# Kernel optimization log

Hardware: AMD Instinct MI355X
Metric: run time of the kernel (lower is better)

Reference implementation:

```python
import jax, jax.numpy as jnp
import numpy as np

NUM_HEADS = 16
D_K = 8  # == n_qubits


def setup_inputs() -> dict:
    key = jax.random.key(0)
    k1, k2, k3 = jax.random.split(key, 3)
    x = jax.random.normal(k1, (4, 2048, 128), dtype=jnp.float32)
    # trainable RX angles, one per qubit (tq.RX has_params=True)
    theta = jax.random.normal(k2, (D_K,), dtype=jnp.float32)
    # out_proj: Linear(embed_dim, embed_dim, bias=False)
    w_out = jax.random.normal(k3, (128, 128), dtype=jnp.float32) * (1.0 / np.sqrt(128.0))
    return {"x": x, "theta": theta, "w_out": w_out}


def quantum_features(x, theta):
    # x: [b, s, e]. Per head of size d_k: encode RX(x_i), trainable RX(theta_i)
    # (composes to RX(x_i + theta_i)), CNOT ladder [i, i+1], measure PauliZ.
    # Heisenberg picture: Z_w -> Z_0...Z_w, so <Z_w> = prod_{i<=w} cos(x_i + theta_i).
    b, s, e = x.shape
    heads = x.reshape(b, s, NUM_HEADS, D_K)
    return jnp.cumprod(jnp.cos(heads + theta), axis=-1)  # [b, s, h, d_k]


def reference(x, theta, w_out):
    b, s, e = x.shape
    # q == k == v: same shared q_layer applied to the same x three times.
    qkv = quantum_features(x, theta)            # [b, s, h, d_k]
    q = qkv.transpose(0, 2, 1, 3)               # [b, h, s, d_k]
    scores = jnp.einsum('bhqd,bhkd->bhqk', q, q) / np.sqrt(D_K)
    attn = jax.nn.softmax(scores, axis=-1)      # dropout is identity at eval
    out = jnp.einsum('bhqk,bhkd->bhqd', attn, q)
    out = out.transpose(0, 2, 1, 3).reshape(b, s, e)
    return out @ w_out.T
```

## Files before the change

kernel.cpp:

```cpp
#include <hip/hip_runtime.h>

#define BATCH 4
#define SEQ   2048
#define EMB   128
#define NH    16
#define DK    8

#define QSCALE 0.510069726f

typedef _Float16 v4h __attribute__((ext_vector_type(4)));
typedef _Float16 v8h __attribute__((ext_vector_type(8)));
typedef float    v4f __attribute__((ext_vector_type(4)));

#define CHUNK 1024
#define VTP   1032

__global__ void feat_kernel(const float* __restrict__ x,
                            const float* __restrict__ theta,
                            _Float16* __restrict__ Fh,
                            _Float16* __restrict__ Qh) {
  __shared__ float Xs[32][132];

  const int tid = threadIdx.x;
  const int b   = blockIdx.x >> 6;
  const int s0  = (blockIdx.x & 63) * 32;

#pragma unroll
  for (int it = 0; it < 4; ++it) {
    const int idx = it * 256 + tid;
    const int r  = idx >> 5;
    const int e4 = idx & 31;
    const float4 v = *(const float4*)(x + ((size_t)b * SEQ + s0 + r) * EMB + e4 * 4);
    *(float4*)&Xs[r][e4 * 4] = v;
  }

  float th[DK];
#pragma unroll
  for (int i = 0; i < DK; ++i) th[i] = theta[i];
  __syncthreads();

#pragma unroll
  for (int it = 0; it < 2; ++it) {
    const int id = it * 256 + tid;
    const int s = id & 31;
    const int h = id >> 5;
    const float* xr = &Xs[s][h * 8];
    const float f0 = __cosf(xr[0] + th[0]);
    const float f1 = f0 * __cosf(xr[1] + th[1]);
    const float f2 = f1 * __cosf(xr[2] + th[2]);
    const float f3 = f2 * __cosf(xr[3] + th[3]);
    const float f4 = f3 * __cosf(xr[4] + th[4]);
    const float f5 = f4 * __cosf(xr[5] + th[5]);
    const float f6 = f5 * __cosf(xr[6] + th[6]);
    const float f7 = f6 * __cosf(xr[7] + th[7]);
    const size_t off = (((size_t)(b * NH + h)) * SEQ + s0 + s) * DK;
    v8h fv = {(_Float16)f0, (_Float16)f1, (_Float16)f2, (_Float16)f3,
              (_Float16)f4, (_Float16)f5, (_Float16)f6, (_Float16)f7};
    v8h qv = {(_Float16)(f0 * QSCALE), (_Float16)(f1 * QSCALE),
              (_Float16)(f2 * QSCALE), (_Float16)(f3 * QSCALE),
              (_Float16)(f4 * QSCALE), (_Float16)(f5 * QSCALE),
              (_Float16)(f6 * QSCALE), (_Float16)(f7 * QSCALE)};
    *(v8h*)(Fh + off) = fv;
    *(v8h*)(Qh + off) = qv;
  }
}

__launch_bounds__(256, 2)
__global__ void attn_kernel(const _Float16* __restrict__ Fh,
                            const _Float16* __restrict__ Qh,
                            float* __restrict__ att ) {
  __shared__ __align__(16) _Float16 Kl[CHUNK * 8];
  __shared__ __align__(16) _Float16 VT[16][VTP];

  const int tid  = threadIdx.x;
  const int L    = tid & 63;
  const int wv   = tid >> 6;
  const int quad = L >> 4;
  const int ln   = L & 15;
  const int bh   = blockIdx.x >> 3;
  const int qb   = (blockIdx.x & 7) * 256 + wv * 64;

  const _Float16* __restrict__ fbase = Fh + (size_t)bh * SEQ * DK;
  const _Float16* __restrict__ qbase = Qh + (size_t)bh * SEQ * DK;

  for (int i = tid; i < 8 * VTP / 4; i += 256) {
    v4h v = (i < VTP / 4) ? (v4h){(_Float16)1.f, (_Float16)1.f,
                                  (_Float16)1.f, (_Float16)1.f}
                          : (v4h){0, 0, 0, 0};
    *(v4h*)(&VT[8][0] + i * 4) = v;
  }

  v4h qf[4];
#pragma unroll
  for (int t = 0; t < 4; ++t) {
    v4h q = {0, 0, 0, 0};
    const int qrow = qb + t * 16 + ln;
    if (quad < 2) q = *(const v4h*)(qbase + (size_t)qrow * DK + quad * 4);
    qf[t] = q;
  }

  v4f acc[4];
#pragma unroll
  for (int t = 0; t < 4; ++t) acc[t] = (v4f){0.f, 0.f, 0.f, 0.f};
  const v4f zf = (v4f){0.f, 0.f, 0.f, 0.f};

  for (int c = 0; c < 2; ++c) {
    if (c) __syncthreads();
    const _Float16* fc = fbase + (size_t)c * CHUNK * DK;
#pragma unroll
    for (int it = 0; it < 4; ++it) {
      const int key = it * 256 + tid;
      *(float4*)&Kl[key * 8] = *(const float4*)(fc + key * 8);
    }
    {
      const int k4 = tid * 4;
      const v8h r0 = *(const v8h*)(fc + (size_t)(k4 + 0) * 8);
      const v8h r1 = *(const v8h*)(fc + (size_t)(k4 + 1) * 8);
      const v8h r2 = *(const v8h*)(fc + (size_t)(k4 + 2) * 8);
      const v8h r3 = *(const v8h*)(fc + (size_t)(k4 + 3) * 8);
#pragma unroll
      for (int d = 0; d < 8; ++d) {
        v4h w = {r0[d], r1[d], r2[d], r3[d]};
        *(v4h*)&VT[d][k4] = w;
      }
    }
    __syncthreads();

    for (int t16 = 0; t16 < CHUNK / 16; ++t16) {
      const v4h kv = *(const v4h*)&Kl[(t16 * 16 + ln) * 8 + (quad & 1) * 4];
      const v4h kf = (quad < 2) ? kv : (v4h){0, 0, 0, 0};
      const v4h vt = *(const v4h*)&VT[ln][t16 * 16 + quad * 4];
#pragma unroll
      for (int t = 0; t < 4; ++t) {
        const v4f s = __builtin_amdgcn_mfma_f32_16x16x16f16(kf, qf[t], zf, 0, 0, 0);
        v4h pb;
        pb[0] = (_Float16)__builtin_amdgcn_exp2f(s[0]);
        pb[1] = (_Float16)__builtin_amdgcn_exp2f(s[1]);
        pb[2] = (_Float16)__builtin_amdgcn_exp2f(s[2]);
        pb[3] = (_Float16)__builtin_amdgcn_exp2f(s[3]);
        acc[t] = __builtin_amdgcn_mfma_f32_16x16x16f16(vt, pb, acc[t], 0, 0, 0);
      }
    }
  }

  const int b = bh >> 4;
  const int h = bh & 15;
#pragma unroll
  for (int t = 0; t < 4; ++t) {
    const float den = __shfl(acc[t][0], 32 + ln, 64);
    const float inv = 1.0f / den;
    if (quad < 2) {
      const int qrow = qb + t * 16 + ln;
      float4 o = make_float4(acc[t][0] * inv, acc[t][1] * inv,
                             acc[t][2] * inv, acc[t][3] * inv);
      *(float4*)(att + ((size_t)b * SEQ + qrow) * EMB + h * DK + quad * 4) = o;
    }
  }
}

__launch_bounds__(256, 1)
__global__ void proj_kernel(float* __restrict__ AO,
                            const float* __restrict__ W) {
  __shared__ float As[64][132];
  __shared__ float Ws[128][132];

  const int tid = threadIdx.x;
  const int tx = tid & 15;
  const int ty = tid >> 4;
  const int rowbase = blockIdx.x * 64;

#pragma unroll
  for (int it = 0; it < 8; ++it) {
    const int idx = it * 256 + tid;
    const int r  = idx >> 5;
    const int e4 = idx & 31;
    *(float4*)&As[r][e4 * 4] =
        *(const float4*)(AO + (size_t)(rowbase + r) * EMB + e4 * 4);
  }
#pragma unroll
  for (int it = 0; it < 16; ++it) {
    const int idx = it * 256 + tid;
    const int n  = idx >> 5;
    const int e4 = idx & 31;
    *(float4*)&Ws[n][e4 * 4] = *(const float4*)(W + (size_t)n * EMB + e4 * 4);
  }
  __syncthreads();

  float acc[4][8] = {{0.f}};

#pragma unroll 2
  for (int e = 0; e < EMB; e += 4) {
    float4 av[4], wvv[8];
#pragma unroll
    for (int i = 0; i < 4; ++i) av[i] = *(const float4*)&As[ty * 4 + i][e];
#pragma unroll
    for (int jj = 0; jj < 8; ++jj) wvv[jj] = *(const float4*)&Ws[tx + 16 * jj][e];
#pragma unroll
    for (int i = 0; i < 4; ++i)
#pragma unroll
      for (int jj = 0; jj < 8; ++jj) {
        acc[i][jj] = fmaf(av[i].x, wvv[jj].x, acc[i][jj]);
        acc[i][jj] = fmaf(av[i].y, wvv[jj].y, acc[i][jj]);
        acc[i][jj] = fmaf(av[i].z, wvv[jj].z, acc[i][jj]);
        acc[i][jj] = fmaf(av[i].w, wvv[jj].w, acc[i][jj]);
      }
  }

#pragma unroll
  for (int i = 0; i < 4; ++i) {
    float* op = AO + (size_t)(rowbase + ty * 4 + i) * EMB;
#pragma unroll
    for (int jj = 0; jj < 8; ++jj) op[tx + 16 * jj] = acc[i][jj];
  }
}

extern "C" void kernel_launch(void* const* d_in, const int* in_sizes, int n_in,
                              void* d_out, int out_size, void* d_ws, size_t ws_size,
                              hipStream_t stream) {
  const float* x     = (const float*)d_in[0];
  const float* theta = (const float*)d_in[1];
  const float* w_out = (const float*)d_in[2];
  float* out = (float*)d_out;
  _Float16* Fh = (_Float16*)d_ws;
  _Float16* Qh = (_Float16*)((char*)d_ws + (size_t)BATCH * NH * SEQ * DK * 2);

  feat_kernel<<<dim3(256), dim3(256), 0, stream>>>(x, theta, Fh, Qh);
  attn_kernel<<<dim3(512), dim3(256), 0, stream>>>(Fh, Qh, out);
  proj_kernel<<<dim3((BATCH * SEQ) / 64), dim3(256), 0, stream>>>(out, w_out);
}
```

Baseline: 110.8 us.

## Use fp16 MFMA for output projection with half-precision attention output and weights

The output projection is rewritten from a scalar fp32 FMA tile loop to 16x16x16 fp16 MFMA instructions. To feed it, the attention kernel now writes its normalized output as fp16 into a workspace buffer, and the feature kernel converts the weight matrix to fp16 as a side task. This halves the intermediate traffic and replaces the VALU-bound projection. In exchange the projection inputs lose precision, and the extra workspace buffers must fit in the provided scratch space.

```diff
diff --git a/kernel.cpp b/kernel.cpp
--- a/kernel.cpp
+++ b/kernel.cpp
@@ -17,8 +17,10 @@
 
 __global__ void feat_kernel(const float* __restrict__ x,
                             const float* __restrict__ theta,
+                            const float* __restrict__ W,
                             _Float16* __restrict__ Fh,
-                            _Float16* __restrict__ Qh) {
+                            _Float16* __restrict__ Qh,
+                            _Float16* __restrict__ Wh) {
   __shared__ float Xs[32][132];
 
   const int tid = threadIdx.x;
@@ -32,6 +34,13 @@
     const int e4 = idx & 31;
     const float4 v = *(const float4*)(x + ((size_t)b * SEQ + s0 + r) * EMB + e4 * 4);
     *(float4*)&Xs[r][e4 * 4] = v;
+  }
+
+  if (tid < 16) {
+    const int i4 = blockIdx.x * 64 + tid * 4;
+    const float4 w = *(const float4*)(W + i4);
+    v4h wh = {(_Float16)w.x, (_Float16)w.y, (_Float16)w.z, (_Float16)w.w};
+    *(v4h*)(Wh + i4) = wh;
   }
 
   float th[DK];
@@ -68,7 +77,7 @@
 __launch_bounds__(256, 2)
 __global__ void attn_kernel(const _Float16* __restrict__ Fh,
                             const _Float16* __restrict__ Qh,
-                            float* __restrict__ att ) {
+                            _Float16* __restrict__ Ah ) {
   __shared__ __align__(16) _Float16 Kl[CHUNK * 8];
   __shared__ __align__(16) _Float16 VT[16][VTP];
 
@@ -151,66 +160,65 @@
     const float inv = 1.0f / den;
     if (quad < 2) {
       const int qrow = qb + t * 16 + ln;
-      float4 o = make_float4(acc[t][0] * inv, acc[t][1] * inv,
-                             acc[t][2] * inv, acc[t][3] * inv);
-      *(float4*)(att + ((size_t)b * SEQ + qrow) * EMB + h * DK + quad * 4) = o;
+      v4h o = {(_Float16)(acc[t][0] * inv), (_Float16)(acc[t][1] * inv),
+               (_Float16)(acc[t][2] * inv), (_Float16)(acc[t][3] * inv)};
+      *(v4h*)(Ah + ((size_t)b * SEQ + qrow) * EMB + h * DK + quad * 4) = o;
     }
   }
 }
 
 __launch_bounds__(256, 1)
-__global__ void proj_kernel(float* __restrict__ AO,
-                            const float* __restrict__ W) {
-  __shared__ float As[64][132];
-  __shared__ float Ws[128][132];
-
-  const int tid = threadIdx.x;
-  const int tx = tid & 15;
-  const int ty = tid >> 4;
+__global__ void proj_kernel(const _Float16* __restrict__ Ah,
+                            const _Float16* __restrict__ Wh,
+                            float* __restrict__ out) {
+  __shared__ __align__(16) _Float16 Ahs[64][136];
+  __shared__ __align__(16) _Float16 Whs[128][136];
+
+  const int tid  = threadIdx.x;
+  const int L    = tid & 63;
+  const int wv   = tid >> 6;
+  const int quad = L >> 4;
+  const int ln   = L & 15;
   const int rowbase = blockIdx.x * 64;
 
+#pragma unroll
+  for (int it = 0; it < 4; ++it) {
+    const int idx = it * 256 + tid;
+    const int r  = idx >> 4;
+    const int c8 = idx & 15;
+    *(uint4*)&Ahs[r][c8 * 8] =
+        *(const uint4*)(Ah + (size_t)(rowbase + r) * EMB + c8 * 8);
+  }
 #pragma unroll
   for (int it = 0; it < 8; ++it) {
     const int idx = it * 256 + tid;
-    const int r  = idx >> 5;
-    const int e4 = idx & 31;
-    *(float4*)&As[r][e4 * 4] =
-        *(const float4*)(AO + (size_t)(rowbase + r) * EMB + e4 * 4);
-  }
-#pragma unroll
-  for (int it = 0; it < 16; ++it) {
-    const int idx = it * 256 + tid;
-    const int n  = idx >> 5;
-    const int e4 = idx & 31;
-    *(float4*)&Ws[n][e4 * 4] = *(const float4*)(W + (size_t)n * EMB + e4 * 4);
+    const int n  = idx >> 4;
+    const int c8 = idx & 15;
+    *(uint4*)&Whs[n][c8 * 8] = *(const uint4*)(Wh + (size_t)n * EMB + c8 * 8);
   }
   __syncthreads();
 
-  float acc[4][8] = {{0.f}};
-
-#pragma unroll 2
-  for (int e = 0; e < EMB; e += 4) {
-    float4 av[4], wvv[8];
-#pragma unroll
-    for (int i = 0; i < 4; ++i) av[i] = *(const float4*)&As[ty * 4 + i][e];
-#pragma unroll
-    for (int jj = 0; jj < 8; ++jj) wvv[jj] = *(const float4*)&Ws[tx + 16 * jj][e];
-#pragma unroll
-    for (int i = 0; i < 4; ++i)
-#pragma unroll
-      for (int jj = 0; jj < 8; ++jj) {
-        acc[i][jj] = fmaf(av[i].x, wvv[jj].x, acc[i][jj]);
-        acc[i][jj] = fmaf(av[i].y, wvv[jj].y, acc[i][jj]);
-        acc[i][jj] = fmaf(av[i].z, wvv[jj].z, acc[i][jj]);
-        acc[i][jj] = fmaf(av[i].w, wvv[jj].w, acc[i][jj]);
-      }
-  }
-
-#pragma unroll
-  for (int i = 0; i < 4; ++i) {
-    float* op = AO + (size_t)(rowbase + ty * 4 + i) * EMB;
-#pragma unroll
-    for (int jj = 0; jj < 8; ++jj) op[tx + 16 * jj] = acc[i][jj];
+  v4f acc[8];
+#pragma unroll
+  for (int nt = 0; nt < 8; ++nt) acc[nt] = (v4f){0.f, 0.f, 0.f, 0.f};
+
+#pragma unroll
+  for (int k8 = 0; k8 < 8; ++k8) {
+    const v4h af = *(const v4h*)&Ahs[wv * 16 + ln][k8 * 16 + quad * 4];
+#pragma unroll
+    for (int nt = 0; nt < 8; ++nt) {
+      const v4h bf = *(const v4h*)&Whs[nt * 16 + ln][k8 * 16 + quad * 4];
+      acc[nt] = __builtin_amdgcn_mfma_f32_16x16x16f16(af, bf, acc[nt], 0, 0, 0);
+    }
+  }
+
+#pragma unroll
+  for (int nt = 0; nt < 8; ++nt) {
+    const int col = nt * 16 + ln;
+#pragma unroll
+    for (int r = 0; r < 4; ++r) {
+      out[(size_t)(rowbase + wv * 16 + quad * 4 + r) * EMB + col] = acc[nt][r];
+    }
   }
 }
 
@@ -221,10 +229,14 @@
   const float* theta = (const float*)d_in[1];
   const float* w_out = (const float*)d_in[2];
   float* out = (float*)d_out;
+
+  const size_t FSZ = (size_t)BATCH * NH * SEQ * DK;
   _Float16* Fh = (_Float16*)d_ws;
-  _Float16* Qh = (_Float16*)((char*)d_ws + (size_t)BATCH * NH * SEQ * DK * 2);
-
-  feat_kernel<<<dim3(256), dim3(256), 0, stream>>>(x, theta, Fh, Qh);
-  attn_kernel<<<dim3(512), dim3(256), 0, stream>>>(Fh, Qh, out);
-  proj_kernel<<<dim3((BATCH * SEQ) / 64), dim3(256), 0, stream>>>(out, w_out);
-}
+  _Float16* Qh = Fh + FSZ;
+  _Float16* Ah = Qh + FSZ;
+  _Float16* Wh = Ah + (size_t)BATCH * SEQ * EMB;
+
+  feat_kernel<<<dim3(256), dim3(256), 0, stream>>>(x, theta, w_out, Fh, Qh, Wh);
+  attn_kernel<<<dim3(512), dim3(256), 0, stream>>>(Fh, Qh, Ah);
+  proj_kernel<<<dim3((BATCH * SEQ) / 64), dim3(256), 0, stream>>>(Ah, Wh, out);
+}
```

Result: faster. 102.9 us (-7.1%).
